# Kernel tuning notes

Measured on AMD Instinct MI355X. Metric: run time of the kernel, lower is better.

The kernel has to match this reference:

```python
import jax, jax.numpy as jnp
import numpy as np

B, H, W, C, G = 256, 64, 64, 3, 128
MH, INV = 10, 18
AS = MH + INV  # 28
EPS = 1e-5


def _bn(x, g, b):
    # training-mode BatchNorm2d: batch stats over (N,H,W), biased variance
    m = x.mean((0, 2, 3), keepdims=True)
    v = x.var((0, 2, 3), keepdims=True)
    return (x - m) * jax.lax.rsqrt(v + EPS) * g.reshape(1, -1, 1, 1) + b.reshape(1, -1, 1, 1)


def _ln(x, g, b):
    m = x.mean(-1, keepdims=True)
    v = x.var(-1, keepdims=True)
    return (x - m) * jax.lax.rsqrt(v + EPS) * g + b


def _conv(x, w, pad):
    return jax.lax.conv_general_dilated(x, w, (1, 1), [(pad, pad), (pad, pad)],
                                        dimension_numbers=('NCHW', 'OIHW', 'NCHW'))


def setup_inputs() -> dict:
    key = jax.random.key(0)
    ks = jax.random.split(key, 24)
    r = lambda i, shape, s=1.0: jax.random.normal(ks[i], shape, jnp.float32) * s
    return {
        'agent_state': r(0, (B, AS)),
        'world_state': r(1, (B, C, H, W)),
        'action': jax.random.uniform(ks[2], (B, 15), jnp.float32, 0.0, 2.999),
        # cnn params
        'bn1_g': jnp.ones((C,), jnp.float32), 'bn1_b': jnp.zeros((C,), jnp.float32),
        'conv1_w': r(3, (G, C, 1, 1), 0.5),
        'bn2_g': jnp.ones((G,), jnp.float32), 'bn2_b': jnp.zeros((G,), jnp.float32),
        'conv2_w': r(4, (G, G, 3, 3), 0.05),
        'bn3_g': jnp.ones((G,), jnp.float32), 'bn3_b': jnp.zeros((G,), jnp.float32),
        'fc1_w': r(5, (20, G), 0.1), 'fc1_b': r(6, (20,), 0.1),
        # mh_inventory
        'ln_mi_g': jnp.ones((AS,), jnp.float32), 'ln_mi_b': jnp.zeros((AS,), jnp.float32),
        'mi_w1': r(7, (100, AS), 0.2), 'mi_w2': r(8, (20, 100), 0.2),
        # action embeddings
        'emb_craft': r(9, (5, 3)), 'emb_equip': r(10, (8, 3)),
        'emb_ncraft': r(11, (8, 3)), 'emb_nsmelt': r(12, (3, 2)), 'emb_place': r(13, (7, 3)),
        # combined_actions
        'ln_ca_g': jnp.ones((24,), jnp.float32), 'ln_ca_b': jnp.zeros((24,), jnp.float32),
        'ca_w1': r(14, (100, 24), 0.2), 'ca_b1': r(15, (100,), 0.1),
        'ca_w2': r(16, (20, 100), 0.2), 'ca_b2': r(17, (20,), 0.1),
        # combined
        'ln_c_g': jnp.ones((60,), jnp.float32), 'ln_c_b': jnp.zeros((60,), jnp.float32),
        'c_w': r(18, (1, 60), 0.2),
        # dist_net
        'ln_d_g': jnp.ones((2 * AS,), jnp.float32), 'ln_d_b': jnp.zeros((2 * AS,), jnp.float32),
        'd_w1': r(19, (50, 2 * AS), 0.2), 'd_w2': r(20, (1, 50), 0.2),
    }


def reference(agent_state, world_state, action,
              bn1_g, bn1_b, conv1_w, bn2_g, bn2_b, conv2_w, bn3_g, bn3_b,
              fc1_w, fc1_b, ln_mi_g, ln_mi_b, mi_w1, mi_w2,
              emb_craft, emb_equip, emb_ncraft, emb_nsmelt, emb_place,
              ln_ca_g, ln_ca_b, ca_w1, ca_b1, ca_w2, ca_b2,
              ln_c_g, ln_c_b, c_w, ln_d_g, ln_d_b, d_w1, d_w2):
    relu = jax.nn.relu
    # ---- CNN branch ----
    x = relu(_bn(world_state, bn1_g, bn1_b))
    x = _conv(x, conv1_w, 0)                      # [B,G,H,W]
    x = relu(_bn(x, bn2_g, bn2_b))
    x = _conv(x, conv2_w, 1)                      # [B,G,H,W]
    x = x.mean((2, 3), keepdims=True)             # AvgPool2d((H,W)) -> [B,G,1,1]
    x = relu(_bn(x, bn3_g, bn3_b)).reshape(x.shape[0], -1)  # [B,G]
    x = relu(x @ fc1_w.T + fc1_b)                 # [B,20]
    # ---- agent-state MLP ----
    y = relu(relu(_ln(agent_state, ln_mi_g, ln_mi_b) @ mi_w1.T) @ mi_w2.T)  # [B,20]
    # ---- per-action embeddings / identities (ModuleDict order) ----
    ai = jax.lax.stop_gradient(action).astype(jnp.int32)
    parts = [action[:, 0:1], action[:, 1:2], action[:, 2:3], action[:, 3:4],
             emb_craft[ai[:, 4]], emb_equip[ai[:, 5]],
             action[:, 6:7], action[:, 7:8], action[:, 8:9],
             emb_ncraft[ai[:, 9]], emb_nsmelt[ai[:, 10]], emb_place[ai[:, 11]],
             action[:, 12:13], action[:, 13:14], action[:, 14:15]]
    acts = jnp.concatenate(parts, axis=1)         # [B,24]
    z = relu(relu(_ln(acts, ln_ca_g, ln_ca_b) @ ca_w1.T + ca_b1) @ ca_w2.T + ca_b2)  # [B,20]
    # ---- combined head ----
    c = jnp.tanh(_ln(jnp.concatenate([x, y, z], axis=1), ln_c_g, ln_c_b) @ c_w.T)    # [B,1]
    # ---- dist_net (previous_agent_state starts as zeros) ----
    prev = jnp.zeros_like(agent_state)
    sc = jnp.concatenate([prev, agent_state], axis=1)  # [B,2*AS]
    d = jnp.tanh(jnp.tanh(_ln(sc, ln_d_g, ln_d_b) @ d_w1.T) @ d_w2.T)                # [B,1]
    return (c, d)
```

## Files before the change

kernel.cpp:

```cpp
#include <hip/hip_runtime.h>
#include <math.h>

#define EPSF 1e-5f

constexpr int OFF_RED1 = 0;
constexpr int OFF_A1B1 = 384;
constexpr int OFF_RED2 = 512;
constexpr int OFF_W2E  = 4096;
constexpr int OFF_M    = OFF_W2E + 128 * 128 * 9;

__device__ __forceinline__ float wave_sum(float v) {
    #pragma unroll
    for (int off = 32; off > 0; off >>= 1) v += __shfl_down(v, off);
    return v;
}

__global__ __launch_bounds__(256) void kA(const float* __restrict__ x,
                                          const float* __restrict__ w2,
                                          float* __restrict__ red1,
                                          float* __restrict__ w2e) {
    int blk = blockIdx.x, tid = threadIdx.x;
    if (blk < 192) {
        int c = blk % 3, seg = blk / 3;
        float s = 0.f, s2 = 0.f;
        for (int bb = 0; bb < 4; ++bb) {
            int b = seg * 4 + bb;
            const float4* p = (const float4*)(x + (size_t)(b * 3 + c) * 4096);
            for (int i = tid; i < 1024; i += 256) {
                float4 v = p[i];
                s += v.x + v.y + v.z + v.w;
                s2 = fmaf(v.x, v.x, s2); s2 = fmaf(v.y, v.y, s2);
                s2 = fmaf(v.z, v.z, s2); s2 = fmaf(v.w, v.w, s2);
            }
        }
        __shared__ float ls[4], ls2[4];
        float ws_ = wave_sum(s), ws2_ = wave_sum(s2);
        if ((tid & 63) == 0) { ls[tid >> 6] = ws_; ls2[tid >> 6] = ws2_; }
        __syncthreads();
        if (tid == 0) {
            red1[blk * 2 + 0] = ls[0] + ls[1] + ls[2] + ls[3];
            red1[blk * 2 + 1] = ls2[0] + ls2[1] + ls2[2] + ls2[3];
        }
    } else {
        int idx = (blk - 192) * 256 + tid;
        int g = idx >> 7, gp = idx & 127;
        const float* wp = w2 + (size_t)(g * 128 + gp) * 9;
        float v0 = wp[0], v1 = wp[1], v2 = wp[2], v3 = wp[3], v4 = wp[4],
              v5 = wp[5], v6 = wp[6], v7 = wp[7], v8 = wp[8];
        float c[9];
        c[0] = ((v0 + v1) + (v2 + v3)) + ((v4 + v5) + (v6 + v7)) + v8;
        c[1] = -(v6 + v7 + v8);
        c[2] = -(v0 + v1 + v2);
        c[3] = -(v2 + v5 + v8);
        c[4] = -(v0 + v3 + v6);
        c[5] = v8; c[6] = v6; c[7] = v2; c[8] = v0;
        #pragma unroll
        for (int k = 0; k < 9; ++k) {
            int jj = gp * 9 + k;
            w2e[(size_t)(jj >> 2) * 512 + g * 4 + (jj & 3)] = c[k];
        }
    }
}

__global__ __launch_bounds__(256) void kB(const float* __restrict__ x,
                                          const float* __restrict__ red1,
                                          const float* __restrict__ g1,
                                          const float* __restrict__ b1,
                                          float* __restrict__ red2,
                                          float* __restrict__ a1b1) {
    __shared__ float ab[6];
    int b = blockIdx.x, tid = threadIdx.x;
    if (tid < 3) {
        float s = 0.f, s2 = 0.f;
        for (int seg = 0; seg < 64; ++seg) {
            s  += red1[(seg * 3 + tid) * 2 + 0];
            s2 += red1[(seg * 3 + tid) * 2 + 1];
        }
        float n = 256.f * 4096.f;
        float mean = s / n, var = s2 / n - mean * mean;
        float a = g1[tid] * rsqrtf(var + EPSF);
        ab[tid] = a; ab[3 + tid] = b1[tid] - mean * a;
        if (b == 0) { a1b1[tid] = a; a1b1[3 + tid] = ab[3 + tid]; }
    }
    __syncthreads();
    float A0 = ab[0], A1 = ab[1], A2 = ab[2];
    float B0 = ab[3], B1 = ab[4], B2 = ab[5];
    float acc[9] = {0, 0, 0, 0, 0, 0, 0, 0, 0};
    const float4* p0 = (const float4*)(x + (size_t)(b * 3 + 0) * 4096);
    const float4* p1 = (const float4*)(x + (size_t)(b * 3 + 1) * 4096);
    const float4* p2 = (const float4*)(x + (size_t)(b * 3 + 2) * 4096);
    for (int i = tid; i < 1024; i += 256) {
        float4 v0 = p0[i], v1 = p1[i], v2 = p2[i];
        #define MOM(e) { \
            float t0 = fmaxf(0.f, fmaf(A0, v0.e, B0)); \
            float t1 = fmaxf(0.f, fmaf(A1, v1.e, B1)); \
            float t2 = fmaxf(0.f, fmaf(A2, v2.e, B2)); \
            acc[0] += t0; acc[1] += t1; acc[2] += t2; \
            acc[3] = fmaf(t0, t0, acc[3]); acc[4] = fmaf(t0, t1, acc[4]); \
            acc[5] = fmaf(t0, t2, acc[5]); acc[6] = fmaf(t1, t1, acc[6]); \
            acc[7] = fmaf(t1, t2, acc[7]); acc[8] = fmaf(t2, t2, acc[8]); }
        MOM(x) MOM(y) MOM(z) MOM(w)
        #undef MOM
    }
    __shared__ float lw[4][9];
    #pragma unroll
    for (int k = 0; k < 9; ++k) {
        float v = wave_sum(acc[k]);
        if ((tid & 63) == 0) lw[tid >> 6][k] = v;
    }
    __syncthreads();
    if (tid == 0) {
        #pragma unroll
        for (int k = 0; k < 9; ++k)
            red2[b * 9 + k] = lw[0][k] + lw[1][k] + lw[2][k] + lw[3][k];
    }
}

__global__ __launch_bounds__(512) void kC(const float* __restrict__ x,
                                          const float* __restrict__ red2,
                                          const float* __restrict__ w1,
                                          const float* __restrict__ g2,
                                          const float* __restrict__ b2,
                                          const float* __restrict__ a1b1,
                                          const float* __restrict__ w2e,
                                          float* __restrict__ m) {
    __shared__ __align__(16) float lds[12288];
    __shared__ __align__(16) float Fsh[1152];
    __shared__ float wt[384], bt[128], momp[288], mom[9], ab[6];
    int b = blockIdx.x, tid = threadIdx.x;
    if (tid < 6) ab[tid] = a1b1[tid];
    if (tid < 288) {
        int seg = tid / 9, k = tid - seg * 9;
        float s = 0.f;
        #pragma unroll
        for (int r = 0; r < 8; ++r) s += red2[(seg * 8 + r) * 9 + k];
        momp[tid] = s;
    }
    __syncthreads();
    if (tid < 9) {
        float s = 0.f;
        #pragma unroll
        for (int sg = 0; sg < 32; ++sg) s += momp[sg * 9 + tid];
        mom[tid] = s / (256.f * 4096.f);
    }
    {
        float A0 = ab[0], A1 = ab[1], A2 = ab[2];
        float B0 = ab[3], B1 = ab[4], B2 = ab[5];
        const float4* xb = (const float4*)(x + (size_t)b * 3 * 4096);
        for (int i = tid; i < 3072; i += 512) {
            float4 v = xb[i];
            int c = i >> 10;
            float a = (c == 0) ? A0 : ((c == 1) ? A1 : A2);
            float bb = (c == 0) ? B0 : ((c == 1) ? B1 : B2);
            v.x = fmaxf(0.f, fmaf(a, v.x, bb));
            v.y = fmaxf(0.f, fmaf(a, v.y, bb));
            v.z = fmaxf(0.f, fmaf(a, v.z, bb));
            v.w = fmaxf(0.f, fmaf(a, v.w, bb));
            *(float4*)&lds[i << 2] = v;
        }
    }
    __syncthreads();
    if (tid < 128) {
        int g = tid;
        float wa = w1[g * 3 + 0], wb = w1[g * 3 + 1], wc = w1[g * 3 + 2];
        float mean = wa * mom[0] + wb * mom[1] + wc * mom[2];
        float ey2 = wa * wa * mom[3] + wb * wb * mom[6] + wc * wc * mom[8]
                  + 2.f * (wa * wb * mom[4] + wa * wc * mom[5] + wb * wc * mom[7]);
        float var = ey2 - mean * mean;
        float a = g2[g] * rsqrtf(var + EPSF);
        wt[g * 3 + 0] = a * wa; wt[g * 3 + 1] = a * wb; wt[g * 3 + 2] = a * wc;
        bt[g] = b2[g] - mean * a;
    }
    __syncthreads();
    int gl = tid & 31, q = tid >> 5;
    {
        float w0[4], w1v[4], w2v[4], bw[4], S[4] = {0, 0, 0, 0};
        #pragma unroll
        for (int j = 0; j < 4; ++j) {
            int g = gl + 32 * j;
            w0[j] = wt[g * 3 + 0]; w1v[j] = wt[g * 3 + 1];
            w2v[j] = wt[g * 3 + 2]; bw[j] = bt[g];
        }
        int base = q * 256;
        #pragma unroll 4
        for (int i = 0; i < 64; ++i) {
            int pp = base + i * 4;
            float4 t0 = *(const float4*)&lds[pp];
            float4 t1 = *(const float4*)&lds[4096 + pp];
            float4 t2 = *(const float4*)&lds[8192 + pp];
            #pragma unroll
            for (int j = 0; j < 4; ++j) {
                float u0 = fmaxf(0.f, fmaf(w0[j], t0.x, fmaf(w1v[j], t1.x, fmaf(w2v[j], t2.x, bw[j]))));
                float u1 = fmaxf(0.f, fmaf(w0[j], t0.y, fmaf(w1v[j], t1.y, fmaf(w2v[j], t2.y, bw[j]))));
                float u2 = fmaxf(0.f, fmaf(w0[j], t0.z, fmaf(w1v[j], t1.z, fmaf(w2v[j], t2.z, bw[j]))));
                float u3 = fmaxf(0.f, fmaf(w0[j], t0.w, fmaf(w1v[j], t1.w, fmaf(w2v[j], t2.w, bw[j]))));
                S[j] += (u0 + u1) + (u2 + u3);
            }
        }
        {
            int g = tid & 127, task = tid >> 7;
            float vw0 = wt[g * 3 + 0], vw1 = wt[g * 3 + 1], vw2 = wt[g * 3 + 2], vb = bt[g];
            float s = 0.f, first = 0.f, last = 0.f;
            int p0 = (task == 1) ? 63 * 64 : ((task == 3) ? 63 : 0);
            int stp = (task >= 2) ? 64 : 1;
            #pragma unroll 4
            for (int i = 0; i < 64; ++i) {
                int p = p0 + i * stp;
                float u = fmaxf(0.f, fmaf(vw0, lds[p], fmaf(vw1, lds[4096 + p], fmaf(vw2, lds[8192 + p], vb))));
                s += u;
                if (i == 0) first = u;
                if (i == 63) last = u;
            }
            Fsh[g * 9 + 1 + task] = s;
            if (task == 0) { Fsh[g * 9 + 5] = first; Fsh[g * 9 + 6] = last; }
            if (task == 1) { Fsh[g * 9 + 7] = first; Fsh[g * 9 + 8] = last; }
        }
        __syncthreads();
        #pragma unroll
        for (int j = 0; j < 4; ++j) lds[(gl + 32 * j) * 17 + q] = S[j];
    }
    __syncthreads();
    if (tid < 128) {
        float s = 0.f;
        #pragma unroll
        for (int qq = 0; qq < 16; ++qq) s += lds[tid * 17 + qq];
        Fsh[tid * 9 + 0] = s;
    }
    __syncthreads();
    {
        int chunk = tid >> 7, g = tid & 127;
        float acc = 0.f;
        #pragma unroll 4
        for (int t = 0; t < 72; ++t) {
            int jb = chunk * 72 + t;
            float4 wv = *(const float4*)&w2e[(size_t)jb * 512 + g * 4];
            float4 fv = *(const float4*)&Fsh[jb * 4];
            acc = fmaf(wv.x, fv.x, fmaf(wv.y, fv.y, fmaf(wv.z, fv.z, fmaf(wv.w, fv.w, acc))));
        }
        __syncthreads();
        lds[chunk * 128 + g] = acc;
    }
    __syncthreads();
    if (tid < 128)
        m[b * 128 + tid] = (lds[tid] + lds[128 + tid] + lds[256 + tid] + lds[384 + tid]) * (1.f / 4096.f);
}

__global__ __launch_bounds__(256) void kE(
    const float* __restrict__ m, const float* __restrict__ g3, const float* __restrict__ b3,
    const float* __restrict__ agent, const float* __restrict__ action,
    const float* __restrict__ fc1w, const float* __restrict__ fc1b,
    const float* __restrict__ lnmig, const float* __restrict__ lnmib,
    const float* __restrict__ miw1, const float* __restrict__ miw2,
    const float* __restrict__ embc, const float* __restrict__ embe,
    const float* __restrict__ embnc, const float* __restrict__ embns,
    const float* __restrict__ embp,
    const float* __restrict__ lncag, const float* __restrict__ lncab,
    const float* __restrict__ caw1, const float* __restrict__ cab1,
    const float* __restrict__ caw2, const float* __restrict__ cab2,
    const float* __restrict__ lncg, const float* __restrict__ lncb,
    const float* __restrict__ cw,
    const float* __restrict__ lndg, const float* __restrict__ lndb,
    const float* __restrict__ dw1, const float* __restrict__ dw2,
    float* __restrict__ out) {
    __shared__ float red[4][128];
    __shared__ float xsh[128];
    __shared__ float lnv[28], lnca[24], lnsc[56], h1[100], h2[100], h3[50], cat[60];
    int b = blockIdx.x, tid = threadIdx.x;
    {
        int g = tid & 127, half = tid >> 7;
        float s = 0.f, s2 = 0.f;
        for (int i = 0; i < 128; ++i) {
            float v = m[(half * 128 + i) * 128 + g];
            s += v; s2 = fmaf(v, v, s2);
        }
        red[half * 2 + 0][g] = s;
        red[half * 2 + 1][g] = s2;
    }
    __syncthreads();
    if (tid < 128) {
        float s = red[0][tid] + red[2][tid], s2 = red[1][tid] + red[3][tid];
        float mean = s / 256.f, var = s2 / 256.f - mean * mean;
        float a = g3[tid] * rsqrtf(var + EPSF);
        float bb = b3[tid] - mean * a;
        xsh[tid] = fmaxf(0.f, fmaf(a, m[b * 128 + tid], bb));
    }
    int l = tid & 63, w = tid >> 6;
    if (w == 0) {
        float av = (l < 28) ? agent[b * 28 + l] : 0.f;
        float s = wave_sum(av), s2 = wave_sum(av * av);
        s = __shfl(s, 0); s2 = __shfl(s2, 0);
        float mean = s / 28.f, var = s2 / 28.f - mean * mean;
        float rs = rsqrtf(var + EPSF);
        if (l < 28) lnv[l] = (av - mean) * rs * lnmig[l] + lnmib[l];
    } else if (w == 1) {
        const float* ab = action + b * 15;
        float actv = 0.f;
        if (l < 24) {
            if (l < 4)       actv = ab[l];
            else if (l < 7)  { int ix = (int)ab[4];  actv = embc[ix * 3 + (l - 4)]; }
            else if (l < 10) { int ix = (int)ab[5];  actv = embe[ix * 3 + (l - 7)]; }
            else if (l < 13) actv = ab[l - 4];
            else if (l < 16) { int ix = (int)ab[9];  actv = embnc[ix * 3 + (l - 13)]; }
            else if (l < 18) { int ix = (int)ab[10]; actv = embns[ix * 2 + (l - 16)]; }
            else if (l < 21) { int ix = (int)ab[11]; actv = embp[ix * 3 + (l - 18)]; }
            else             actv = ab[l - 9];
        }
        float s = wave_sum(actv), s2 = wave_sum(actv * actv);
        s = __shfl(s, 0); s2 = __shfl(s2, 0);
        float mean = s / 24.f, var = s2 / 24.f - mean * mean;
        float rs = rsqrtf(var + EPSF);
        if (l < 24) lnca[l] = (actv - mean) * rs * lncag[l] + lncab[l];
    } else if (w == 2) {
        float g1v = (l < 56) ? agent[b * 28 + (l < 28 ? l : l - 28)] : 0.f;
        float av = (l < 28) ? g1v : 0.f;
        float s = wave_sum(av), s2 = wave_sum(av * av);
        s = __shfl(s, 0); s2 = __shfl(s2, 0);
        float mean = s / 56.f, var = s2 / 56.f - mean * mean;
        float rs = rsqrtf(var + EPSF);
        if (l < 56) {
            float vv = (l < 28) ? 0.f : g1v;
            lnsc[l] = (vv - mean) * rs * lndg[l] + lndb[l];
        }
    }
    __syncthreads();
    if (tid < 100) {
        float a = 0.f;
        for (int i = 0; i < 28; ++i) a = fmaf(miw1[tid * 28 + i], lnv[i], a);
        h1[tid] = fmaxf(0.f, a);
    } else if (tid < 200) {
        int j = tid - 100;
        float a = cab1[j];
        for (int i = 0; i < 24; ++i) a = fmaf(caw1[j * 24 + i], lnca[i], a);
        h2[j] = fmaxf(0.f, a);
    } else if (tid < 250) {
        int j = tid - 200;
        float a = 0.f;
        for (int i = 0; i < 56; ++i) a = fmaf(dw1[j * 56 + i], lnsc[i], a);
        h3[j] = tanhf(a);
    }
    __syncthreads();
    if (tid < 20) {
        float a = 0.f;
        for (int i = 0; i < 100; ++i) a = fmaf(miw2[tid * 100 + i], h1[i], a);
        cat[20 + tid] = fmaxf(0.f, a);
    } else if (tid >= 64 && tid < 84) {
        int j = tid - 64;
        float a = cab2[j];
        for (int i = 0; i < 100; ++i) a = fmaf(caw2[j * 100 + i], h2[i], a);
        cat[40 + j] = fmaxf(0.f, a);
    } else if (tid >= 128 && tid < 148) {
        int j = tid - 128;
        float a = fc1b[j];
        for (int i = 0; i < 128; ++i) a = fmaf(fc1w[j * 128 + i], xsh[i], a);
        cat[j] = fmaxf(0.f, a);
    } else if (tid >= 192) {
        int l3 = tid - 192;
        float dt = (l3 < 50) ? dw2[l3] * h3[l3] : 0.f;
        dt = wave_sum(dt);
        if (l3 == 0) out[256 + b] = tanhf(dt);
    }
    __syncthreads();
    if (w == 0) {
        float cv = (l < 60) ? cat[l] : 0.f;
        float ss = wave_sum(cv), ss2 = wave_sum(cv * cv);
        ss = __shfl(ss, 0); ss2 = __shfl(ss2, 0);
        float mean60 = ss / 60.f, var60 = ss2 / 60.f - mean60 * mean60;
        float rs60 = rsqrtf(var60 + EPSF);
        float term = (l < 60) ? cw[l] * ((cv - mean60) * rs60 * lncg[l] + lncb[l]) : 0.f;
        term = wave_sum(term);
        if (l == 0) out[b] = tanhf(term);
    }
}

extern "C" void kernel_launch(void* const* d_in, const int* in_sizes, int n_in,
                              void* d_out, int out_size, void* d_ws, size_t ws_size,
                              hipStream_t stream) {
    (void)in_sizes; (void)n_in; (void)out_size; (void)ws_size;
    const float* agent  = (const float*)d_in[0];
    const float* world  = (const float*)d_in[1];
    const float* action = (const float*)d_in[2];
    const float* bn1_g  = (const float*)d_in[3];
    const float* bn1_b  = (const float*)d_in[4];
    const float* conv1w = (const float*)d_in[5];
    const float* bn2_g  = (const float*)d_in[6];
    const float* bn2_b  = (const float*)d_in[7];
    const float* conv2w = (const float*)d_in[8];
    const float* bn3_g  = (const float*)d_in[9];
    const float* bn3_b  = (const float*)d_in[10];
    const float* fc1w   = (const float*)d_in[11];
    const float* fc1b   = (const float*)d_in[12];
    const float* lnmig  = (const float*)d_in[13];
    const float* lnmib  = (const float*)d_in[14];
    const float* miw1   = (const float*)d_in[15];
    const float* miw2   = (const float*)d_in[16];
    const float* embc   = (const float*)d_in[17];
    const float* embe   = (const float*)d_in[18];
    const float* embnc  = (const float*)d_in[19];
    const float* embns  = (const float*)d_in[20];
    const float* embp   = (const float*)d_in[21];
    const float* lncag  = (const float*)d_in[22];
    const float* lncab  = (const float*)d_in[23];
    const float* caw1   = (const float*)d_in[24];
    const float* cab1   = (const float*)d_in[25];
    const float* caw2   = (const float*)d_in[26];
    const float* cab2   = (const float*)d_in[27];
    const float* lncg   = (const float*)d_in[28];
    const float* lncb   = (const float*)d_in[29];
    const float* cw     = (const float*)d_in[30];
    const float* lndg   = (const float*)d_in[31];
    const float* lndb   = (const float*)d_in[32];
    const float* dw1    = (const float*)d_in[33];
    const float* dw2    = (const float*)d_in[34];
    float* out = (float*)d_out;
    float* ws = (float*)d_ws;

    hipLaunchKernelGGL(kA, dim3(256), dim3(256), 0, stream,
                       world, conv2w, ws + OFF_RED1, ws + OFF_W2E);
    hipLaunchKernelGGL(kB, dim3(256), dim3(256), 0, stream,
                       world, ws + OFF_RED1, bn1_g, bn1_b, ws + OFF_RED2, ws + OFF_A1B1);
    hipLaunchKernelGGL(kC, dim3(256), dim3(512), 0, stream,
                       world, ws + OFF_RED2, conv1w, bn2_g, bn2_b, ws + OFF_A1B1,
                       ws + OFF_W2E, ws + OFF_M);
    hipLaunchKernelGGL(kE, dim3(256), dim3(256), 0, stream,
                       ws + OFF_M, bn3_g, bn3_b, agent, action, fc1w, fc1b,
                       lnmig, lnmib, miw1, miw2,
                       embc, embe, embnc, embns, embp,
                       lncag, lncab, caw1, cab1, caw2, cab2,
                       lncg, lncb, cw, lndg, lndb, dw1, dw2, out);
}
```

Measured before the change: 187.3 us.

## Split conv kernel across two blocks per image by output-channel half

The fused conv1/conv2 kernel now launches two 256-thread blocks per image, each handling 64 of the 128 intermediate channels, instead of one 512-thread block. Each half writes partial conv2 means to separate buffers, and the head kernel sums the two partials. The per-thread inner loop now covers 8 channels over 32 pixel groups, with a staggered start index to spread LDS accesses. This doubles the block count to raise occupancy. In exchange, each block loads the full input image into LDS again, and the head kernel reads an extra partial buffer.

Measured after the change: 190.5 us. Within noise of the previous version (+1.7%).

```diff
diff --git a/kernel.cpp b/kernel.cpp
--- a/kernel.cpp
+++ b/kernel.cpp
@@ -7,7 +7,8 @@
 constexpr int OFF_A1B1 = 384;
 constexpr int OFF_RED2 = 512;
 constexpr int OFF_W2E  = 4096;
-constexpr int OFF_M    = OFF_W2E + 128 * 128 * 9;
+constexpr int OFF_M0   = OFF_W2E + 128 * 128 * 9;
+constexpr int OFF_M1   = OFF_M0 + 256 * 128;
 
 __device__ __forceinline__ float wave_sum(float v) {
     #pragma unroll
@@ -116,42 +117,45 @@
     }
 }
 
-__global__ __launch_bounds__(512) void kC(const float* __restrict__ x,
+__global__ __launch_bounds__(256) void kC(const float* __restrict__ x,
                                           const float* __restrict__ red2,
                                           const float* __restrict__ w1,
                                           const float* __restrict__ g2,
                                           const float* __restrict__ b2,
                                           const float* __restrict__ a1b1,
                                           const float* __restrict__ w2e,
-                                          float* __restrict__ m) {
+                                          float* __restrict__ mp0,
+                                          float* __restrict__ mp1) {
     __shared__ __align__(16) float lds[12288];
-    __shared__ __align__(16) float Fsh[1152];
-    __shared__ float wt[384], bt[128], momp[288], mom[9], ab[6];
-    int b = blockIdx.x, tid = threadIdx.x;
+    __shared__ __align__(16) float Fsh[576];
+    __shared__ float wt[192], bt[64], momp[144], mom[9], ab[6];
+    int b = blockIdx.x >> 1, h = blockIdx.x & 1, tid = threadIdx.x;
     if (tid < 6) ab[tid] = a1b1[tid];
-    if (tid < 288) {
-        int seg = tid / 9, k = tid - seg * 9;
+    if (tid >= 64 && tid < 208) {
+        int t = tid - 64;
+        int seg = t / 9, k = t - seg * 9;
         float s = 0.f;
         #pragma unroll
-        for (int r = 0; r < 8; ++r) s += red2[(seg * 8 + r) * 9 + k];
-        momp[tid] = s;
+        for (int r = 0; r < 16; ++r) s += red2[(seg * 16 + r) * 9 + k];
+        momp[t] = s;
     }
     __syncthreads();
     if (tid < 9) {
         float s = 0.f;
         #pragma unroll
-        for (int sg = 0; sg < 32; ++sg) s += momp[sg * 9 + tid];
+        for (int sg = 0; sg < 16; ++sg) s += momp[sg * 9 + tid];
         mom[tid] = s / (256.f * 4096.f);
     }
     {
         float A0 = ab[0], A1 = ab[1], A2 = ab[2];
         float B0 = ab[3], B1 = ab[4], B2 = ab[5];
-        const float4* xb = (const float4*)(x + (size_t)b * 3 * 4096);
-        for (int i = tid; i < 3072; i += 512) {
+        const float4* xb = (const float4*)(x + (size_t)b * 12288);
+        #pragma unroll
+        for (int k = 0; k < 12; ++k) {
+            int i = k * 256 + tid;
             float4 v = xb[i];
-            int c = i >> 10;
-            float a = (c == 0) ? A0 : ((c == 1) ? A1 : A2);
-            float bb = (c == 0) ? B0 : ((c == 1) ? B1 : B2);
+            float a = (k < 4) ? A0 : ((k < 8) ? A1 : A2);
+            float bb = (k < 4) ? B0 : ((k < 8) ? B1 : B2);
             v.x = fmaxf(0.f, fmaf(a, v.x, bb));
             v.y = fmaxf(0.f, fmaf(a, v.y, bb));
             v.z = fmaxf(0.f, fmaf(a, v.z, bb));
@@ -160,36 +164,38 @@
         }
     }
     __syncthreads();
-    if (tid < 128) {
-        int g = tid;
+    if (tid < 64) {
+        int g = h * 64 + tid;
         float wa = w1[g * 3 + 0], wb = w1[g * 3 + 1], wc = w1[g * 3 + 2];
         float mean = wa * mom[0] + wb * mom[1] + wc * mom[2];
         float ey2 = wa * wa * mom[3] + wb * wb * mom[6] + wc * wc * mom[8]
                   + 2.f * (wa * wb * mom[4] + wa * wc * mom[5] + wb * wc * mom[7]);
         float var = ey2 - mean * mean;
         float a = g2[g] * rsqrtf(var + EPSF);
-        wt[g * 3 + 0] = a * wa; wt[g * 3 + 1] = a * wb; wt[g * 3 + 2] = a * wc;
-        bt[g] = b2[g] - mean * a;
-    }
-    __syncthreads();
-    int gl = tid & 31, q = tid >> 5;
+        wt[tid * 3 + 0] = a * wa; wt[tid * 3 + 1] = a * wb; wt[tid * 3 + 2] = a * wc;
+        bt[tid] = b2[g] - mean * a;
+    }
+    __syncthreads();
+    int gl = tid & 7, q = tid >> 3;
     {
-        float w0[4], w1v[4], w2v[4], bw[4], S[4] = {0, 0, 0, 0};
-        #pragma unroll
-        for (int j = 0; j < 4; ++j) {
-            int g = gl + 32 * j;
+        float w0[8], w1v[8], w2v[8], bw[8], S[8];
+        #pragma unroll
+        for (int j = 0; j < 8; ++j) {
+            int g = gl + 8 * j;
             w0[j] = wt[g * 3 + 0]; w1v[j] = wt[g * 3 + 1];
             w2v[j] = wt[g * 3 + 2]; bw[j] = bt[g];
-        }
-        int base = q * 256;
+            S[j] = 0.f;
+        }
+        int stag = (q & 7) * 4;
         #pragma unroll 4
-        for (int i = 0; i < 64; ++i) {
-            int pp = base + i * 4;
-            float4 t0 = *(const float4*)&lds[pp];
-            float4 t1 = *(const float4*)&lds[4096 + pp];
-            float4 t2 = *(const float4*)&lds[8192 + pp];
+        for (int i = 0; i < 32; ++i) {
+            int ie = (i + stag) & 31;
+            int px = q * 128 + ie * 4;
+            float4 t0 = *(const float4*)&lds[px];
+            float4 t1 = *(const float4*)&lds[4096 + px];
+            float4 t2 = *(const float4*)&lds[8192 + px];
             #pragma unroll
-            for (int j = 0; j < 4; ++j) {
+            for (int j = 0; j < 8; ++j) {
                 float u0 = fmaxf(0.f, fmaf(w0[j], t0.x, fmaf(w1v[j], t1.x, fmaf(w2v[j], t2.x, bw[j]))));
                 float u1 = fmaxf(0.f, fmaf(w0[j], t0.y, fmaf(w1v[j], t1.y, fmaf(w2v[j], t2.y, bw[j]))));
                 float u2 = fmaxf(0.f, fmaf(w0[j], t0.z, fmaf(w1v[j], t1.z, fmaf(w2v[j], t2.z, bw[j]))));
@@ -198,15 +204,15 @@
             }
         }
         {
-            int g = tid & 127, task = tid >> 7;
+            int g = tid & 63, task = tid >> 6;
             float vw0 = wt[g * 3 + 0], vw1 = wt[g * 3 + 1], vw2 = wt[g * 3 + 2], vb = bt[g];
             float s = 0.f, first = 0.f, last = 0.f;
             int p0 = (task == 1) ? 63 * 64 : ((task == 3) ? 63 : 0);
             int stp = (task >= 2) ? 64 : 1;
             #pragma unroll 4
             for (int i = 0; i < 64; ++i) {
-                int p = p0 + i * stp;
-                float u = fmaxf(0.f, fmaf(vw0, lds[p], fmaf(vw1, lds[4096 + p], fmaf(vw2, lds[8192 + p], vb))));
+                int px = p0 + i * stp;
+                float u = fmaxf(0.f, fmaf(vw0, lds[px], fmaf(vw1, lds[4096 + px], fmaf(vw2, lds[8192 + px], vb))));
                 s += u;
                 if (i == 0) first = u;
                 if (i == 63) last = u;
@@ -217,36 +223,40 @@
         }
         __syncthreads();
         #pragma unroll
-        for (int j = 0; j < 4; ++j) lds[(gl + 32 * j) * 17 + q] = S[j];
-    }
-    __syncthreads();
-    if (tid < 128) {
+        for (int j = 0; j < 8; ++j) lds[(gl + 8 * j) * 33 + q] = S[j];
+    }
+    __syncthreads();
+    if (tid < 64) {
         float s = 0.f;
         #pragma unroll
-        for (int qq = 0; qq < 16; ++qq) s += lds[tid * 17 + qq];
+        for (int qq = 0; qq < 32; ++qq) s += lds[tid * 33 + qq];
         Fsh[tid * 9 + 0] = s;
     }
     __syncthreads();
     {
         int chunk = tid >> 7, g = tid & 127;
         float acc = 0.f;
+        int jb0 = h * 144 + chunk * 72;
         #pragma unroll 4
         for (int t = 0; t < 72; ++t) {
-            int jb = chunk * 72 + t;
+            int jb = jb0 + t;
             float4 wv = *(const float4*)&w2e[(size_t)jb * 512 + g * 4];
-            float4 fv = *(const float4*)&Fsh[jb * 4];
+            float4 fv = *(const float4*)&Fsh[(chunk * 72 + t) * 4];
             acc = fmaf(wv.x, fv.x, fmaf(wv.y, fv.y, fmaf(wv.z, fv.z, fmaf(wv.w, fv.w, acc))));
         }
         __syncthreads();
         lds[chunk * 128 + g] = acc;
     }
     __syncthreads();
-    if (tid < 128)
-        m[b * 128 + tid] = (lds[tid] + lds[128 + tid] + lds[256 + tid] + lds[384 + tid]) * (1.f / 4096.f);
+    if (tid < 128) {
+        float* mp = h ? mp1 : mp0;
+        mp[b * 128 + tid] = (lds[tid] + lds[128 + tid]) * (1.f / 4096.f);
+    }
 }
 
 __global__ __launch_bounds__(256) void kE(
-    const float* __restrict__ m, const float* __restrict__ g3, const float* __restrict__ b3,
+    const float* __restrict__ mp0, const float* __restrict__ mp1,
+    const float* __restrict__ g3, const float* __restrict__ b3,
     const float* __restrict__ agent, const float* __restrict__ action,
     const float* __restrict__ fc1w, const float* __restrict__ fc1b,
     const float* __restrict__ lnmig, const float* __restrict__ lnmib,
@@ -270,7 +280,8 @@
         int g = tid & 127, half = tid >> 7;
         float s = 0.f, s2 = 0.f;
         for (int i = 0; i < 128; ++i) {
-            float v = m[(half * 128 + i) * 128 + g];
+            int idx = (half * 128 + i) * 128 + g;
+            float v = mp0[idx] + mp1[idx];
             s += v; s2 = fmaf(v, v, s2);
         }
         red[half * 2 + 0][g] = s;
@@ -282,7 +293,8 @@
         float mean = s / 256.f, var = s2 / 256.f - mean * mean;
         float a = g3[tid] * rsqrtf(var + EPSF);
         float bb = b3[tid] - mean * a;
-        xsh[tid] = fmaxf(0.f, fmaf(a, m[b * 128 + tid], bb));
+        float mv = mp0[b * 128 + tid] + mp1[b * 128 + tid];
+        xsh[tid] = fmaxf(0.f, fmaf(a, mv, bb));
     }
     int l = tid & 63, w = tid >> 6;
     if (w == 0) {
@@ -418,11 +430,11 @@
                        world, conv2w, ws + OFF_RED1, ws + OFF_W2E);
     hipLaunchKernelGGL(kB, dim3(256), dim3(256), 0, stream,
                        world, ws + OFF_RED1, bn1_g, bn1_b, ws + OFF_RED2, ws + OFF_A1B1);
-    hipLaunchKernelGGL(kC, dim3(256), dim3(512), 0, stream,
+    hipLaunchKernelGGL(kC, dim3(512), dim3(256), 0, stream,
                        world, ws + OFF_RED2, conv1w, bn2_g, bn2_b, ws + OFF_A1B1,
-                       ws + OFF_W2E, ws + OFF_M);
+                       ws + OFF_W2E, ws + OFF_M0, ws + OFF_M1);
     hipLaunchKernelGGL(kE, dim3(256), dim3(256), 0, stream,
-                       ws + OFF_M, bn3_g, bn3_b, agent, action, fc1w, fc1b,
+                       ws + OFF_M0, ws + OFF_M1, bn3_g, bn3_b, agent, action, fc1w, fc1b,
                        lnmig, lnmib, miw1, miw2,
                        embc, embe, embnc, embns, embp,
                        lncag, lncab, caw1, cab1, caw2, cab2,
```
